# Optimization experiments

Measured on AMD Instinct MI355X. Metric: run time of the kernel, lower is better.

Reference implementation:

```python
import jax, jax.numpy as jnp
import numpy as np

NUM_HEADS = 8  # config.num_heads


def setup_inputs() -> dict:
    key = jax.random.key(0)
    k0, k1, k2, k3, k4 = jax.random.split(key, 5)
    B, N, C, E = 32, 20000, 8, 512
    query_embeddings = jax.random.normal(k0, (B, E), dtype=jnp.float32)
    all_embeddings = jax.random.normal(k1, (N, E), dtype=jnp.float32)
    label_mask = jax.random.bernoulli(k2, 0.5, (N, C))  # bool multi-label mask
    # per-class MultiheadAttention q/k in-projection params (torch Linear convention: x @ W.T + b)
    Wq = jax.random.normal(k3, (C, E, E), dtype=jnp.float32) * 0.02
    Wk = jax.random.normal(k4, (C, E, E), dtype=jnp.float32) * 0.02
    bq = jnp.zeros((C, E), dtype=jnp.float32)
    bk = jnp.zeros((C, E), dtype=jnp.float32)
    return {
        "query_embeddings": query_embeddings,
        "all_embeddings": all_embeddings,
        "label_mask": label_mask,
        "Wq": Wq,
        "bq": bq,
        "Wk": Wk,
        "bk": bk,
        "n_samples": 5,
    }


def reference(query_embeddings, all_embeddings, label_mask, Wq, bq, Wk, bk, n_samples):
    """Vectorized-over-classes version of EmbeddingSelector.get_similar_samples.

    For each class c: q = query @ Wq[c].T + bq[c]; k_c over the class's database
    members; per-head scaled-dot softmax; attn weights averaged over heads
    (torch MHA need_weights default); top-k over class members. Non-members are
    masked to -inf before softmax, so they get weight 0 and (since every class
    has >> n_samples members) never enter the top-k -- identical math to the
    per-class gather loop, with global indices returned directly.
    """
    C, E, _ = Wq.shape
    H = NUM_HEADS
    dh = E // H
    B = query_embeddings.shape[0]
    N = all_embeddings.shape[0]

    # per-class projections (torch Linear: x @ W.T + b)
    q = jnp.einsum('be,cfe->cbf', query_embeddings, Wq) + bq[:, None, :]   # (C,B,E)
    k = jnp.einsum('ne,cfe->cnf', all_embeddings, Wk) + bk[:, None, :]     # (C,N,E)
    q = q.reshape(C, B, H, dh)
    k = k.reshape(C, N, H, dh)

    scale = 1.0 / jnp.sqrt(jnp.asarray(dh, q.dtype))
    scores = jnp.einsum('cbhd,cnhd->cbhn', q, k) * scale                   # (C,B,H,N)
    member = jnp.transpose(label_mask)[:, None, None, :]                   # (C,1,1,N)
    scores = jnp.where(member, scores, jnp.asarray(-1e9, scores.dtype))
    attn = jax.nn.softmax(scores, axis=-1).mean(axis=2)                    # (C,B,N) head-avg

    weights, indices = jax.lax.top_k(attn, n_samples)                      # (C,B,ns)
    result_weights = jnp.transpose(weights, (1, 0, 2))                     # (B,C,ns)
    result_indices = jnp.transpose(indices, (1, 0, 2)).astype(jnp.int32)   # (B,C,ns) global ids
    return result_indices, result_weights
```

## Files before the change

### kernel.cpp

```cpp
#include <hip/hip_runtime.h>
#include <math.h>

#define B_  32
#define N_  20000
#define C_  8
#define E_  512
#define H_  8
#define SCALE 0.125f
#define UNSC  9.765625e-4f

#define CHUNK 1024
#define NCH   20
#define NC3   157
#define SSZ ((size_t)B_ * H_ * N_)

typedef __attribute__((ext_vector_type(8))) _Float16 h8_t;
typedef __attribute__((ext_vector_type(4))) float f32x4;

#define MFMAH(a, b, c) __builtin_amdgcn_mfma_f32_16x16x32_f16(a, b, c, 0, 0, 0)

__device__ inline unsigned short f16_round(float x, float& fv) {
    _Float16 h = (_Float16)x;
    fv = (float)h;
    union { _Float16 hh; unsigned short us; } u;
    u.hh = h;
    return u.us;
}

__global__ __launch_bounds__(256) void k_q2(
        const float* __restrict__ x, const float* __restrict__ Wq,
        const float* __restrict__ bq, float* __restrict__ q) {
    int ft = blockIdx.x, c = blockIdx.y;
    int f0 = ft * 8;
    __shared__ float wsm[8][66];
    __shared__ float xs[32][66];
    int tid = threadIdx.x;
    int b = tid & 31, fs = tid >> 5;
    float acc = 0.f;
    const float* W = Wq + (size_t)c * E_ * E_;
    for (int k0 = 0; k0 < E_; k0 += 64) {
        __syncthreads();
        for (int i = tid; i < 512; i += 256)
            wsm[i >> 6][i & 63] = W[(size_t)(f0 + (i >> 6)) * E_ + k0 + (i & 63)];
        for (int i = tid; i < 2048; i += 256)
            xs[i >> 6][i & 63] = x[(size_t)(i >> 6) * E_ + k0 + (i & 63)];
        __syncthreads();
        #pragma unroll
        for (int kk = 0; kk < 64; ++kk)
            acc += xs[b][kk] * wsm[fs][kk];
    }
    q[((size_t)c * B_ + b) * E_ + f0 + fs] = acc + bq[c * E_ + f0 + fs];
}

__global__ __launch_bounds__(256) void k_u2(
        const float* __restrict__ q, const float* __restrict__ Wk,
        const float* __restrict__ bk, float* __restrict__ u,
        float* __restrict__ qb) {
    int et = blockIdx.x, h = blockIdx.y, c = blockIdx.z;
    int e0 = et * 64;
    __shared__ float qs[32][66];
    __shared__ float wk[64][66];
    int tid = threadIdx.x;
    int b = tid & 31, es = tid >> 5;
    for (int i = tid; i < 2048; i += 256)
        qs[i >> 6][i & 63] = q[((size_t)c * B_ + (i >> 6)) * E_ + h * 64 + (i & 63)];
    const float* W = Wk + (size_t)c * E_ * E_ + (size_t)(h * 64) * E_;
    for (int i = tid; i < 4096; i += 256)
        wk[i >> 6][i & 63] = W[(size_t)(i >> 6) * E_ + e0 + (i & 63)];
    __syncthreads();
    float acc[8] = {};
    for (int d = 0; d < 64; ++d) {
        float qv = qs[b][d];
        #pragma unroll
        for (int j = 0; j < 8; ++j)
            acc[j] += qv * wk[d][es * 8 + j];
    }
    float* urow = u + ((size_t)c * 256 + b * 8 + h) * E_ + e0 + es * 8;
    #pragma unroll
    for (int j = 0; j < 8; ++j) urow[j] = acc[j];
    if (et == 0 && es == 0) {
        float s = 0.f;
        const float* bkr = bk + c * E_ + h * 64;
        for (int d = 0; d < 64; ++d) s += qs[b][d] * bkr[d];
        qb[c * 256 + b * 8 + h] = s;
    }
}

#define U2P ((size_t)C_ * 16 * 16 * 512)

__global__ void k_split_u2(const float* __restrict__ u, short* __restrict__ u2) {
    int bx = blockIdx.x;
    int ks = bx & 15, mt = (bx >> 4) & 15, c = bx >> 8;
    int lane = threadIdx.x;
    int m  = mt * 16 + (lane & 15);
    int k0 = ks * 32 + (lane >> 4) * 8;
    const float* up = u + ((size_t)c * 256 + m) * 512 + k0;
    size_t base = ((((size_t)c * 16 + mt) * 16 + ks) * 512) + (size_t)lane * 8;
    #pragma unroll
    for (int j = 0; j < 8; ++j) {
        float x = up[j] * 32.0f, fh, fm;
        unsigned short h = f16_round(x, fh);
        unsigned short mm = f16_round(x - fh, fm);
        u2[base + j]       = (short)h;
        u2[U2P + base + j] = (short)mm;
    }
}

__global__ void k_split_A2(const float* __restrict__ A, short* __restrict__ A2t) {
    int nc = blockIdx.x, ks = blockIdx.y;
    int tid = threadIdx.x;
    int n = tid >> 1, kg = (tid & 1) * 2;
    int gn = nc * 128 + n;
    const float* ap = A + (size_t)gn * 512 + ks * 32 + kg * 8;
    short vh[2][8], vm[2][8];
    #pragma unroll
    for (int g = 0; g < 2; ++g)
        #pragma unroll
        for (int j = 0; j < 8; ++j) {
            float x = (gn < N_) ? ap[g * 8 + j] * 32.0f : 0.f;
            float fh, fm;
            vh[g][j] = (short)f16_round(x, fh);
            vm[g][j] = (short)f16_round(x - fh, fm);
        }
    short* outp = A2t + ((size_t)nc * 16 + ks) * 8192 + n * 32;
    #pragma unroll
    for (int g = 0; g < 2; ++g) {
        int p = ((kg + g) + (n >> 1)) & 3;
        #pragma unroll
        for (int j = 0; j < 8; ++j) {
            outp[p * 8 + j]        = vh[g][j];
            outp[4096 + p * 8 + j] = vm[g][j];
        }
    }
}

__global__ __launch_bounds__(256, 2) void k_scores_mfma(
        const short* __restrict__ u2, const short* __restrict__ A2t,
        const float* __restrict__ qb, const int* __restrict__ mask,
        float* __restrict__ S, float* __restrict__ Zpart, int c0, int CB) {
    __shared__ __align__(16) short As[16384];
    __shared__ float sQb[256];
    __shared__ int   sMask[128];
    int bx = blockIdx.x;
    int z  = bx % CB;
    int c  = c0 + z;
    int nc = bx / CB;
    int tid = threadIdx.x;
    int lane = tid & 63, w = tid >> 6;
    int quad = lane >> 4, l15 = lane & 15;
    int n0 = nc * 128;

    sQb[tid] = qb[c * 256 + tid];
    if (tid < 128) {
        int n = n0 + tid;
        sMask[tid] = (n < N_) ? mask[(size_t)n * C_ + c] : 0;
    }

    f32x4 acc[4][8];
    #pragma unroll
    for (int i = 0; i < 4; ++i)
        #pragma unroll
        for (int j = 0; j < 8; ++j)
            acc[i][j] = (f32x4){0.f, 0.f, 0.f, 0.f};

    const float4* tb = (const float4*)((const char*)A2t + (size_t)nc * 262144);

    for (int ks2 = 0; ks2 < 8; ++ks2) {
        __syncthreads();
        const float4* src = tb + ks2 * 2048;
        float4* dst = (float4*)As;
        #pragma unroll
        for (int t = 0; t < 8; ++t) dst[tid + t * 256] = src[tid + t * 256];
        __syncthreads();

        #pragma unroll
        for (int kh = 0; kh < 2; ++kh) {
            int ks = ks2 * 2 + kh;
            const short* Ab = As + kh * 8192;
            h8_t af[4][2];
            #pragma unroll
            for (int mt = 0; mt < 4; ++mt) {
                size_t ub = ((((size_t)c * 16 + (w * 4 + mt)) * 16 + ks) * 512)
                            + (size_t)lane * 8;
                af[mt][0] = *(const h8_t*)(u2 + ub);
                af[mt][1] = *(const h8_t*)(u2 + U2P + ub);
            }
            #pragma unroll
            for (int nt = 0; nt < 8; ++nt) {
                int r = nt * 16 + l15;
                const short* bp = Ab + r * 32 + ((quad + (r >> 1)) & 3) * 8;
                h8_t b0 = *(const h8_t*)bp;
                h8_t b1 = *(const h8_t*)(bp + 4096);
                #pragma unroll
                for (int mt = 0; mt < 4; ++mt) {
                    f32x4 a = acc[mt][nt];
                    a = MFMAH(af[mt][0], b0, a);
                    a = MFMAH(af[mt][0], b1, a);
                    a = MFMAH(af[mt][1], b0, a);
                    acc[mt][nt] = a;
                }
            }
        }
    }

    float* Sc = S + (size_t)z * SSZ;
    #pragma unroll
    for (int mt = 0; mt < 4; ++mt) {
        float rs[4] = {0.f, 0.f, 0.f, 0.f};
        #pragma unroll
        for (int nt = 0; nt < 8; ++nt) {
            int nl = nt * 16 + l15;
            int n = n0 + nl;
            int mem = sMask[nl];
            #pragma unroll
            for (int r = 0; r < 4; ++r) {
                int m = w * 64 + mt * 16 + quad * 4 + r;
                float sc = SCALE * (acc[mt][nt][r] * UNSC + sQb[m]);
                float ev = mem ? __expf(sc) : 0.f;
                rs[r] += ev;
                if (n < N_) Sc[(size_t)m * N_ + n] = ev;
            }
        }
        #pragma unroll
        for (int r = 0; r < 4; ++r) {
            float v = rs[r];
            v += __shfl_xor(v, 1); v += __shfl_xor(v, 2);
            v += __shfl_xor(v, 4); v += __shfl_xor(v, 8);
            if (l15 == 0) {
                int m = w * 64 + mt * 16 + quad * 4 + r;
                Zpart[((size_t)nc * C_ + c) * 256 + m] = v;
            }
        }
    }
}

__global__ void k_zsum(const float* __restrict__ Zpart, float* __restrict__ Z, int c0) {
    int c = c0 + blockIdx.x;
    int i = c * 256 + threadIdx.x;
    float s = 0.f;
    for (int nc = 0; nc < NC3; ++nc) s += Zpart[(size_t)nc * (C_ * 256) + i];
    Z[i] = s;
}

__global__ __launch_bounds__(256) void k_topk1(
        const float* __restrict__ S, const float* __restrict__ Z,
        float2* __restrict__ cand, int c0, int ns) {
    int chunk = blockIdx.x, b = blockIdx.y, z = blockIdx.z;
    const float* Sc = S + (size_t)z * SSZ;
    int tid = threadIdx.x;
    __shared__ float zr[H_];
    if (tid < H_) zr[tid] = 1.0f / Z[(c0 + z) * (B_ * H_) + b * H_ + tid];
    __syncthreads();
    int n0 = chunk * CHUNK + tid * 4;
    bool valid = n0 < N_;
    float4 a = make_float4(0.f, 0.f, 0.f, 0.f);
    if (valid) {
        #pragma unroll
        for (int h = 0; h < H_; ++h) {
            const float4 sv = *(const float4*)&Sc[(size_t)(b * H_ + h) * N_ + n0];
            float wz = zr[h];
            a.x += sv.x * wz; a.y += sv.y * wz; a.z += sv.z * wz; a.w += sv.w * wz;
        }
    }
    float v[4]; int ix[4];
    v[0] = valid ? a.x * 0.125f : -1.f;
    v[1] = valid ? a.y * 0.125f : -1.f;
    v[2] = valid ? a.z * 0.125f : -1.f;
    v[3] = valid ? a.w * 0.125f : -1.f;
    #pragma unroll
    for (int t = 0; t < 4; ++t) ix[t] = valid ? n0 + t : N_;

    __shared__ float wv[4];
    __shared__ int   wi[4];
    __shared__ int   winS;
    int lane = tid & 63, w = tid >> 6;
    for (int j = 0; j < ns; ++j) {
        float bv = v[0]; int bi = ix[0];
        #pragma unroll
        for (int t = 1; t < 4; ++t)
            if (v[t] > bv || (v[t] == bv && ix[t] < bi)) { bv = v[t]; bi = ix[t]; }
        #pragma unroll
        for (int off = 1; off < 64; off <<= 1) {
            float ov = __shfl_xor(bv, off, 64);
            int   oi = __shfl_xor(bi, off, 64);
            if (ov > bv || (ov == bv && oi < bi)) { bv = ov; bi = oi; }
        }
        if (lane == 0) { wv[w] = bv; wi[w] = bi; }
        __syncthreads();
        if (tid == 0) {
            float fv = wv[0]; int fi = wi[0];
            #pragma unroll
            for (int t = 1; t < 4; ++t)
                if (wv[t] > fv || (wv[t] == fv && wi[t] < fi)) { fv = wv[t]; fi = wi[t]; }
            cand[(((size_t)z * B_ + b) * NCH + chunk) * ns + j] =
                make_float2(fv, (float)fi);
            winS = fi;
        }
        __syncthreads();
        int wn = winS;
        #pragma unroll
        for (int t = 0; t < 4; ++t)
            if (ix[t] == wn) v[t] = -2.f;
    }
}

__global__ __launch_bounds__(256) void k_topk2(
        const float2* __restrict__ cand, float* __restrict__ out, int c0, int ns) {
    int b = blockIdx.x, z = blockIdx.y;
    int c = c0 + z;
    int tid = threadIdx.x;
    int ncand = NCH * ns;
    const float2* cb = cand + ((size_t)z * B_ + b) * ncand;
    float v = -3.f; int ix = N_ + 1;
    if (tid < ncand) { float2 e = cb[tid]; v = e.x; ix = (int)e.y; }
    __shared__ float sv[256];
    __shared__ int   si[256];
    __shared__ int   win;
    for (int j = 0; j < ns; ++j) {
        sv[tid] = v; si[tid] = ix;
        __syncthreads();
        for (int w = 128; w >= 1; w >>= 1) {
            if (tid < w) {
                float v2 = sv[tid + w]; int i2 = si[tid + w];
                if (v2 > sv[tid] || (v2 == sv[tid] && i2 < si[tid])) {
                    sv[tid] = v2; si[tid] = i2;
                }
            }
            __syncthreads();
        }
        if (tid == 0) {
            out[((size_t)b * C_ + c) * ns + j] = (float)si[0];
            out[(size_t)B_ * C_ * ns + ((size_t)b * C_ + c) * ns + j] = sv[0];
            win = si[0];
        }
        __syncthreads();
        if (ix == win) v = -3.f;
        __syncthreads();
    }
}

extern "C" void kernel_launch(void* const* d_in, const int* in_sizes, int n_in,
                              void* d_out, int out_size, void* d_ws, size_t ws_size,
                              hipStream_t stream) {
    const float* x    = (const float*)d_in[0];
    const float* A    = (const float*)d_in[1];
    const int*   mask = (const int*)  d_in[2];
    const float* Wq   = (const float*)d_in[3];
    const float* bq   = (const float*)d_in[4];
    const float* Wk   = (const float*)d_in[5];
    const float* bk   = (const float*)d_in[6];
    float* out = (float*)d_out;

    int ns = out_size / (2 * B_ * C_);

    float* ws = (float*)d_ws;
    float* q     = ws;
    float* u     = q     + (size_t)C_ * B_ * E_;
    float* qb    = u     + (size_t)C_ * B_ * H_ * E_;
    float* Z     = qb    + (size_t)C_ * B_ * H_;
    float* Zpart = Z     + (size_t)C_ * B_ * H_;
    short* u2    = (short*)(Zpart + (size_t)NC3 * C_ * 256);
    short* A2t   = u2 + 2 * U2P;
    float* S     = (float*)(A2t + (size_t)NC3 * 16 * 8192);
    size_t fixedFloats = (size_t)(S - ws);

    size_t candFloats = (size_t)C_ * B_ * NCH * ns * 2;
    int CB = 8;
    while (CB > 1 &&
           (fixedFloats + (size_t)CB * SSZ + candFloats + 16) * 4 > ws_size)
        CB >>= 1;
    float2* cand = (float2*)(S + (size_t)CB * SSZ);

    k_q2<<<dim3(64, C_), 256, 0, stream>>>(x, Wq, bq, q);
    k_u2<<<dim3(8, H_, C_), 256, 0, stream>>>(q, Wk, bk, u, qb);
    k_split_u2<<<C_ * 16 * 16, 64, 0, stream>>>(u, u2);
    k_split_A2<<<dim3(NC3, 16), 256, 0, stream>>>(A, A2t);

    for (int c0 = 0; c0 < C_; c0 += CB) {
        k_scores_mfma<<<NC3 * CB, 256, 0, stream>>>(u2, A2t, qb, mask, S, Zpart, c0, CB);
        k_zsum<<<CB, 256, 0, stream>>>(Zpart, Z, c0);
        k_topk1<<<dim3(NCH, B_, CB), 256, 0, stream>>>(S, Z, cand, c0, ns);
        k_topk2<<<dim3(B_, CB), 256, 0, stream>>>(cand, out, c0, ns);
    }
}
```

Baseline: 395.9 us.

## Use direct global-to-LDS loads, vectorize split stores, and remap score blocks

The scores kernel now fills shared memory with global_load_lds 16-byte direct transfers, so tile data no longer passes through registers. Its block index is remapped so that groups of eight consecutive chunks share a class, padding the grid to 20×8 per class and returning early for out-of-range chunks, which may change L2 locality for the A2t tiles. The split kernels now write their fp16 hi/lo outputs as 8-wide vector stores instead of scalar stores. The direct-to-LDS path requires the intrinsic's layout to match the existing swizzle, and the padded blocks add a few idle launches.

Measured after the change: 388.8 us. Within noise of the previous version (-1.8%).

```diff
diff --git a/kernel.cpp b/kernel.cpp
--- a/kernel.cpp
+++ b/kernel.cpp
@@ -12,12 +12,19 @@
 #define CHUNK 1024
 #define NCH   20
 #define NC3   157
+#define NCG   20
 #define SSZ ((size_t)B_ * H_ * N_)
 
 typedef __attribute__((ext_vector_type(8))) _Float16 h8_t;
+typedef __attribute__((ext_vector_type(8))) short   s8_t;
 typedef __attribute__((ext_vector_type(4))) float f32x4;
 
 #define MFMAH(a, b, c) __builtin_amdgcn_mfma_f32_16x16x32_f16(a, b, c, 0, 0, 0)
+
+#define GLOAD_LDS16(g, l)                                              \
+    __builtin_amdgcn_global_load_lds(                                  \
+        (const __attribute__((address_space(1))) unsigned int*)(g),    \
+        (__attribute__((address_space(3))) unsigned int*)(l), 16, 0, 0)
 
 __device__ inline unsigned short f16_round(float x, float& fv) {
     _Float16 h = (_Float16)x;
@@ -96,14 +103,15 @@
     int k0 = ks * 32 + (lane >> 4) * 8;
     const float* up = u + ((size_t)c * 256 + m) * 512 + k0;
     size_t base = ((((size_t)c * 16 + mt) * 16 + ks) * 512) + (size_t)lane * 8;
+    s8_t vh, vm;
     #pragma unroll
     for (int j = 0; j < 8; ++j) {
         float x = up[j] * 32.0f, fh, fm;
-        unsigned short h = f16_round(x, fh);
-        unsigned short mm = f16_round(x - fh, fm);
-        u2[base + j]       = (short)h;
-        u2[U2P + base + j] = (short)mm;
-    }
+        vh[j] = (short)f16_round(x, fh);
+        vm[j] = (short)f16_round(x - fh, fm);
+    }
+    *(s8_t*)(u2 + base)       = vh;
+    *(s8_t*)(u2 + U2P + base) = vm;
 }
 
 __global__ void k_split_A2(const float* __restrict__ A, short* __restrict__ A2t) {
@@ -112,7 +120,7 @@
     int n = tid >> 1, kg = (tid & 1) * 2;
     int gn = nc * 128 + n;
     const float* ap = A + (size_t)gn * 512 + ks * 32 + kg * 8;
-    short vh[2][8], vm[2][8];
+    s8_t vh[2], vm[2];
     #pragma unroll
     for (int g = 0; g < 2; ++g)
         #pragma unroll
@@ -126,11 +134,8 @@
     #pragma unroll
     for (int g = 0; g < 2; ++g) {
         int p = ((kg + g) + (n >> 1)) & 3;
-        #pragma unroll
-        for (int j = 0; j < 8; ++j) {
-            outp[p * 8 + j]        = vh[g][j];
-            outp[4096 + p * 8 + j] = vm[g][j];
-        }
+        *(s8_t*)(outp + p * 8)        = vh[g];
+        *(s8_t*)(outp + 4096 + p * 8) = vm[g];
     }
 }
 
@@ -142,9 +147,13 @@
     __shared__ float sQb[256];
     __shared__ int   sMask[128];
     int bx = blockIdx.x;
-    int z  = bx % CB;
+    int x    = bx & 7;
+    int rest = bx >> 3;
+    int z    = rest % CB;
+    int g    = rest / CB;
+    int nc   = g * 8 + x;
+    if (nc >= NC3) return;
     int c  = c0 + z;
-    int nc = bx / CB;
     int tid = threadIdx.x;
     int lane = tid & 63, w = tid >> 6;
     int quad = lane >> 4, l15 = lane & 15;
@@ -163,14 +172,17 @@
         for (int j = 0; j < 8; ++j)
             acc[i][j] = (f32x4){0.f, 0.f, 0.f, 0.f};
 
-    const float4* tb = (const float4*)((const char*)A2t + (size_t)nc * 262144);
+    const char* tb = (const char*)A2t + (size_t)nc * 262144;
 
     for (int ks2 = 0; ks2 < 8; ++ks2) {
         __syncthreads();
-        const float4* src = tb + ks2 * 2048;
-        float4* dst = (float4*)As;
-        #pragma unroll
-        for (int t = 0; t < 8; ++t) dst[tid + t * 256] = src[tid + t * 256];
+        const char* src = tb + (size_t)ks2 * 32768;
+        #pragma unroll
+        for (int t = 0; t < 8; ++t) {
+            int seg = w * 8 + t;
+            GLOAD_LDS16(src + (size_t)seg * 1024 + lane * 16,
+                        (char*)As + seg * 1024);
+        }
         __syncthreads();
 
         #pragma unroll
@@ -377,7 +389,7 @@
     k_split_A2<<<dim3(NC3, 16), 256, 0, stream>>>(A, A2t);
 
     for (int c0 = 0; c0 < C_; c0 += CB) {
-        k_scores_mfma<<<NC3 * CB, 256, 0, stream>>>(u2, A2t, qb, mask, S, Zpart, c0, CB);
+        k_scores_mfma<<<NCG * 8 * CB, 256, 0, stream>>>(u2, A2t, qb, mask, S, Zpart, c0, CB);
         k_zsum<<<CB, 256, 0, stream>>>(Zpart, Z, c0);
         k_topk1<<<dim3(NCH, B_, CB), 256, 0, stream>>>(S, Z, cand, c0, ns);
         k_topk2<<<dim3(B_, CB), 256, 0, stream>>>(cand, out, c0, ns);
```
